# Performance work log

Measured on AMD Instinct MI355X. Metric: run time of the kernel, lower is better.

The kernel has to match this reference:

```python
import jax, jax.numpy as jnp
import numpy as np

BETA = 0.01  # soft-threshold level (init kwarg)
EPS = 1e-12


def vector_to_toeplitz(v):
    # v: [2N-1] complex generator; T[i, j] = v[N-1 + i - j], shape [N, N]
    n = (v.shape[0] + 1) // 2
    ii = jnp.arange(n)[:, None]
    jj = jnp.arange(n)[None, :]
    return v[(n - 1) + ii - jj]


def soft_thresh(z, beta):
    # complex soft-threshold (proximal op of beta*||.||_1):
    # z * max(|z| - beta, 0) / |z|
    mag = jnp.abs(z)
    scale = jnp.maximum(mag - beta, 0.0) / jnp.maximum(mag, EPS)
    return z * scale.astype(z.real.dtype)


def setup_inputs() -> dict:
    key = jax.random.key(0)
    ks = jax.random.split(key, 8)
    N, M, B = 1024, 256, 1024
    d = jnp.float32
    return {
        "v_re": jax.random.normal(ks[0], (2 * N - 1,), d),
        "v_im": jax.random.normal(ks[1], (2 * N - 1,), d),
        "W2_re": jax.random.normal(ks[2], (N, M), d) / np.sqrt(M),
        "W2_im": jax.random.normal(ks[3], (N, M), d) / np.sqrt(M),
        "x_re": jax.random.normal(ks[4], (N, B), d),
        "x_im": jax.random.normal(ks[5], (N, B), d),
        "y_re": jax.random.normal(ks[6], (M, B), d),
        "y_im": jax.random.normal(ks[7], (M, B), d),
    }


def reference(v_re, v_im, W2_re, W2_im, x_re, x_im, y_re, y_im):
    v = jax.lax.complex(v_re, v_im)      # [2N-1]
    W2 = jax.lax.complex(W2_re, W2_im)   # [N, M] (= A^H)
    x = jax.lax.complex(x_re, x_im)      # [N, B]
    y = jax.lax.complex(y_re, y_im)      # [M, B]
    W1 = vector_to_toeplitz(v)           # [N, N] Toeplitz
    # tpm(W1, x) + W2 @ y, then complex soft-threshold
    z = soft_thresh(W1 @ x + W2 @ y, BETA)  # [N, B]
    return z
```

## Files before the change

### kernel.cpp

```cpp
#include <hip/hip_runtime.h>
#include <hip/hip_fp16.h>
#include <cstdint>
#include <cstddef>


#define K_DIM 2560
#define BETA_F 0.01f
#define EPS_F  1e-12f

typedef __attribute__((ext_vector_type(8))) _Float16 half8;
typedef __attribute__((ext_vector_type(4))) _Float16 half4;
typedef __attribute__((ext_vector_type(4))) float   floatx4;

__device__ alignas(16) _Float16 g_Ap[1024 * K_DIM];
__device__ alignas(16) _Float16 g_Bt[2048 * K_DIM];
__device__ alignas(16) float    g_P0[1024 * 2048];
__device__ alignas(16) float    g_P1[1024 * 2048];

__global__ __launch_bounds__(256) void build_A(
    const float* __restrict__ v_re, const float* __restrict__ v_im,
    const float* __restrict__ W2_re, const float* __restrict__ W2_im)
{
    int t = blockIdx.x * 256 + threadIdx.x;
    int i  = t / 320;
    int c  = t - i * 320;
    int kp = c * 8;
    half8 h;
    if (kp < 1024) {
#pragma unroll
        for (int j = 0; j < 8; ++j) h[j] = (_Float16)v_re[1023 + i - kp - j];
    } else if (kp < 1280) {
        const float* s = W2_re + i * 256 + (kp - 1024);
#pragma unroll
        for (int j = 0; j < 8; ++j) h[j] = (_Float16)s[j];
    } else if (kp < 2304) {
        int k2 = kp - 1280;
#pragma unroll
        for (int j = 0; j < 8; ++j) h[j] = (_Float16)v_im[1023 + i - k2 - j];
    } else {
        const float* s = W2_im + i * 256 + (kp - 2304);
#pragma unroll
        for (int j = 0; j < 8; ++j) h[j] = (_Float16)s[j];
    }
    *reinterpret_cast<half8*>(g_Ap + (size_t)i * K_DIM + kp) = h;
}

__global__ __launch_bounds__(256) void build_Bt(
    const float* __restrict__ x_re, const float* __restrict__ x_im,
    const float* __restrict__ y_re, const float* __restrict__ y_im)
{
    __shared__ float lre[32][33];
    __shared__ float lim[32][33];
    int tid = threadIdx.x;
    int tx = tid & 31, ty = tid >> 5;
    int bx = blockIdx.x;
    const float* sre = (bx < 32) ? x_re : y_re;
    const float* sim = (bx < 32) ? x_im : y_im;
    int kb   = (bx < 32) ? bx : (bx - 32);
    int koff = (bx < 32) ? 0 : 1024;
    int k0 = kb * 32;
    int n0 = blockIdx.y * 32;
#pragma unroll
    for (int s = 0; s < 4; ++s) {
        int kk = ty + 8 * s;
        lre[kk][tx] = sre[(size_t)(k0 + kk) * 1024 + n0 + tx];
        lim[kk][tx] = sim[(size_t)(k0 + kk) * 1024 + n0 + tx];
    }
    __syncthreads();
    int lane_n = tid >> 3;
    int kq     = (tid & 7) * 4;
    half4 hre, him, hmim;
#pragma unroll
    for (int j = 0; j < 4; ++j) {
        float re = lre[kq + j][lane_n];
        float im = lim[kq + j][lane_n];
        hre[j]  = (_Float16)re;
        him[j]  = (_Float16)im;
        hmim[j] = (_Float16)(-im);
    }
    int n = n0 + lane_n;
    size_t kk2 = (size_t)koff + k0 + kq;
    _Float16* r0 = g_Bt + (size_t)(2 * n)     * K_DIM;
    _Float16* r1 = g_Bt + (size_t)(2 * n + 1) * K_DIM;
    *reinterpret_cast<half4*>(r0 + kk2)        = hre;
    *reinterpret_cast<half4*>(r0 + kk2 + 1280) = hmim;
    *reinterpret_cast<half4*>(r1 + kk2)        = him;
    *reinterpret_cast<half4*>(r1 + kk2 + 1280) = hre;
}

__global__ __launch_bounds__(256) void gemm_split(void)
{
    __shared__ __align__(16) _Float16 As[2 * 2 * 64 * 32];
    __shared__ __align__(16) _Float16 Bs[2 * 2 * 64 * 32];

    const int tid  = threadIdx.x;
    const int lane = tid & 63;
    const int w    = tid >> 6;
    const int wm   = w >> 1;
    const int wn   = w & 1;

    const int bid   = blockIdx.x;
    const int split = bid >> 9;
    const int sb    = bid & 511;
    const int xcd   = sb & 7;
    const int t     = sb >> 3;
    const int mi0 = ((xcd & 1) * 8 + (t & 7)) * 64;
    const int ni0 = ((xcd >> 1) * 8 + (t >> 3)) * 64;
    const int ks  = split * 1280;
    float* __restrict__ P = split ? g_P1 : g_P0;

    floatx4 acc[2][2];
#pragma unroll
    for (int a = 0; a < 2; ++a)
#pragma unroll
        for (int b = 0; b < 2; ++b) acc[a][b] = (floatx4)0.0f;

    const int rS = tid >> 2;
    const int jS = tid & 3;
    const int s0 = ((rS & 15) >> 1) & 3;
    char* asW = (char*)As + rS * 64 + ((jS ^ s0) * 16);
    char* bsW = (char*)Bs + rS * 64 + ((jS ^ s0) * 16);
    const _Float16* gA = g_Ap + (size_t)(mi0 + rS) * K_DIM + ks + jS * 8;
    const _Float16* gB = g_Bt + (size_t)(ni0 + rS) * K_DIM + ks + jS * 8;

    const int rowA = lane & 15;
    const int q    = lane >> 4;
    const int coff = (q ^ ((rowA >> 1) & 3)) * 16;

    {
        half8 pA0 = *reinterpret_cast<const half8*>(gA);
        half8 pA1 = *reinterpret_cast<const half8*>(gA + 32);
        half8 pB0 = *reinterpret_cast<const half8*>(gB);
        half8 pB1 = *reinterpret_cast<const half8*>(gB + 32);
        *reinterpret_cast<half8*>(asW)        = pA0;
        *reinterpret_cast<half8*>(asW + 4096) = pA1;
        *reinterpret_cast<half8*>(bsW)        = pB0;
        *reinterpret_cast<half8*>(bsW + 4096) = pB1;
    }
    __syncthreads();

    const int NIT = 1280 / 64;
    for (int kt = 0; kt < NIT; ++kt) {
        const int cur = kt & 1;
        half8 pA0, pA1, pB0, pB1;
        if (kt < NIT - 1) {
            const _Float16* ga = gA + (kt + 1) * 64;
            const _Float16* gb = gB + (kt + 1) * 64;
            pA0 = *reinterpret_cast<const half8*>(ga);
            pA1 = *reinterpret_cast<const half8*>(ga + 32);
            pB0 = *reinterpret_cast<const half8*>(gb);
            pB1 = *reinterpret_cast<const half8*>(gb + 32);
        }
        const char* Ab = (const char*)As + cur * 8192;
        const char* Bb = (const char*)Bs + cur * 8192;
        half8 af[2][2], bf[2][2];
#pragma unroll
        for (int mi = 0; mi < 2; ++mi) {
            int r = wm * 32 + mi * 16 + rowA;
            af[mi][0] = *reinterpret_cast<const half8*>(Ab + r * 64 + coff);
            af[mi][1] = *reinterpret_cast<const half8*>(Ab + 4096 + r * 64 + coff);
        }
#pragma unroll
        for (int ni = 0; ni < 2; ++ni) {
            int r = wn * 32 + ni * 16 + rowA;
            bf[ni][0] = *reinterpret_cast<const half8*>(Bb + r * 64 + coff);
            bf[ni][1] = *reinterpret_cast<const half8*>(Bb + 4096 + r * 64 + coff);
        }
#pragma unroll
        for (int mi = 0; mi < 2; ++mi)
#pragma unroll
            for (int ni = 0; ni < 2; ++ni) {
                acc[mi][ni] = __builtin_amdgcn_mfma_f32_16x16x32_f16(
                    af[mi][0], bf[ni][0], acc[mi][ni], 0, 0, 0);
                acc[mi][ni] = __builtin_amdgcn_mfma_f32_16x16x32_f16(
                    af[mi][1], bf[ni][1], acc[mi][ni], 0, 0, 0);
            }
        if (kt < NIT - 1) {
            char* aw = asW + (cur ^ 1) * 8192;
            char* bw = bsW + (cur ^ 1) * 8192;
            *reinterpret_cast<half8*>(aw)        = pA0;
            *reinterpret_cast<half8*>(aw + 4096) = pA1;
            *reinterpret_cast<half8*>(bw)        = pB0;
            *reinterpret_cast<half8*>(bw + 4096) = pB1;
        }
        __syncthreads();
    }

    const int colL  = lane & 15;
    const int rquad = (lane >> 4) * 4;
#pragma unroll
    for (int mi = 0; mi < 2; ++mi)
#pragma unroll
        for (int ni = 0; ni < 2; ++ni)
#pragma unroll
            for (int r = 0; r < 4; ++r) {
                int row = mi0 + wm * 32 + mi * 16 + rquad + r;
                int col = ni0 + wn * 32 + ni * 16 + colL;
                P[(size_t)row * 2048 + col] = acc[mi][ni][r];
            }
}

__global__ __launch_bounds__(256) void reduce_soft(float* __restrict__ out,
                                                   int out_n)
{
    int t = blockIdx.x * 256 + threadIdx.x;
    floatx4 v0 = reinterpret_cast<const floatx4*>(g_P0)[t];
    floatx4 v1 = reinterpret_cast<const floatx4*>(g_P1)[t];
    float re0 = v0[0] + v1[0], im0 = v0[1] + v1[1];
    float re1 = v0[2] + v1[2], im1 = v0[3] + v1[3];
    float m0 = sqrtf(re0 * re0 + im0 * im0);
    float m1 = sqrtf(re1 * re1 + im1 * im1);
    float s0 = fmaxf(m0 - BETA_F, 0.0f) / fmaxf(m0, EPS_F);
    float s1 = fmaxf(m1 - BETA_F, 0.0f) / fmaxf(m1, EPS_F);
    float2 r = make_float2(re0 * s0, re1 * s1);
    int idx = t * 2;
    if (idx + 1 < out_n)
        *reinterpret_cast<float2*>(out + idx) = r;
}

extern "C" void kernel_launch(void* const* d_in, const int* in_sizes, int n_in,
                              void* d_out, int out_size, void* d_ws, size_t ws_size,
                              hipStream_t stream) {
    (void)d_ws; (void)ws_size; (void)in_sizes; (void)n_in;
    const float* v_re  = (const float*)d_in[0];
    const float* v_im  = (const float*)d_in[1];
    const float* W2_re = (const float*)d_in[2];
    const float* W2_im = (const float*)d_in[3];
    const float* x_re  = (const float*)d_in[4];
    const float* x_im  = (const float*)d_in[5];
    const float* y_re  = (const float*)d_in[6];
    const float* y_im  = (const float*)d_in[7];
    float* out = (float*)d_out;

    build_A<<<1280, 256, 0, stream>>>(v_re, v_im, W2_re, W2_im);
    build_Bt<<<dim3(40, 32), 256, 0, stream>>>(x_re, x_im, y_re, y_im);
    gemm_split<<<1024, 256, 0, stream>>>();
    reduce_soft<<<2048, 256, 0, stream>>>(out, out_size);
}
```

Measured before the change: 116.9 us.

## Split GEMM K four ways, fuse build kernels, and add occupancy hint

Merges the two operand-building kernels into one launch, which removes one kernel boundary. The GEMM K dimension is split into four pieces instead of two, doubling the grid to 2048 blocks, and the block-to-tile mapping is reordered so that splits of the same tile land on the same XCD. A launch-bounds occupancy hint of 8 is also added. In exchange the partial-sum buffers double in size, so the reduce kernel must read four 8 MB arrays instead of two, which adds memory traffic.

```diff
diff --git a/kernel.cpp b/kernel.cpp
--- a/kernel.cpp
+++ b/kernel.cpp
@@ -14,52 +14,53 @@
 
 __device__ alignas(16) _Float16 g_Ap[1024 * K_DIM];
 __device__ alignas(16) _Float16 g_Bt[2048 * K_DIM];
-__device__ alignas(16) float    g_P0[1024 * 2048];
-__device__ alignas(16) float    g_P1[1024 * 2048];
-
-__global__ __launch_bounds__(256) void build_A(
+__device__ alignas(16) float    g_P[4][1024 * 2048];
+
+__global__ __launch_bounds__(256) void build_all(
     const float* __restrict__ v_re, const float* __restrict__ v_im,
-    const float* __restrict__ W2_re, const float* __restrict__ W2_im)
-{
-    int t = blockIdx.x * 256 + threadIdx.x;
-    int i  = t / 320;
-    int c  = t - i * 320;
-    int kp = c * 8;
-    half8 h;
-    if (kp < 1024) {
-#pragma unroll
-        for (int j = 0; j < 8; ++j) h[j] = (_Float16)v_re[1023 + i - kp - j];
-    } else if (kp < 1280) {
-        const float* s = W2_re + i * 256 + (kp - 1024);
-#pragma unroll
-        for (int j = 0; j < 8; ++j) h[j] = (_Float16)s[j];
-    } else if (kp < 2304) {
-        int k2 = kp - 1280;
-#pragma unroll
-        for (int j = 0; j < 8; ++j) h[j] = (_Float16)v_im[1023 + i - k2 - j];
-    } else {
-        const float* s = W2_im + i * 256 + (kp - 2304);
-#pragma unroll
-        for (int j = 0; j < 8; ++j) h[j] = (_Float16)s[j];
-    }
-    *reinterpret_cast<half8*>(g_Ap + (size_t)i * K_DIM + kp) = h;
-}
-
-__global__ __launch_bounds__(256) void build_Bt(
+    const float* __restrict__ W2_re, const float* __restrict__ W2_im,
     const float* __restrict__ x_re, const float* __restrict__ x_im,
     const float* __restrict__ y_re, const float* __restrict__ y_im)
 {
+    const int bx = blockIdx.x;
+    if (bx < 1280) {
+        int t = bx * 256 + threadIdx.x;
+        int i  = t / 320;
+        int c  = t - i * 320;
+        int kp = c * 8;
+        half8 h;
+        if (kp < 1024) {
+#pragma unroll
+            for (int j = 0; j < 8; ++j) h[j] = (_Float16)v_re[1023 + i - kp - j];
+        } else if (kp < 1280) {
+            const float* s = W2_re + i * 256 + (kp - 1024);
+#pragma unroll
+            for (int j = 0; j < 8; ++j) h[j] = (_Float16)s[j];
+        } else if (kp < 2304) {
+            int k2 = kp - 1280;
+#pragma unroll
+            for (int j = 0; j < 8; ++j) h[j] = (_Float16)v_im[1023 + i - k2 - j];
+        } else {
+            const float* s = W2_im + i * 256 + (kp - 2304);
+#pragma unroll
+            for (int j = 0; j < 8; ++j) h[j] = (_Float16)s[j];
+        }
+        *reinterpret_cast<half8*>(g_Ap + (size_t)i * K_DIM + kp) = h;
+        return;
+    }
     __shared__ float lre[32][33];
     __shared__ float lim[32][33];
+    int idx = bx - 1280;
+    int bk  = idx % 40;
+    int by  = idx / 40;
+    const float* sre = (bk < 32) ? x_re : y_re;
+    const float* sim = (bk < 32) ? x_im : y_im;
+    int kb   = (bk < 32) ? bk : (bk - 32);
+    int koff = (bk < 32) ? 0 : 1024;
+    int k0 = kb * 32;
+    int n0 = by * 32;
     int tid = threadIdx.x;
     int tx = tid & 31, ty = tid >> 5;
-    int bx = blockIdx.x;
-    const float* sre = (bx < 32) ? x_re : y_re;
-    const float* sim = (bx < 32) ? x_im : y_im;
-    int kb   = (bx < 32) ? bx : (bx - 32);
-    int koff = (bx < 32) ? 0 : 1024;
-    int k0 = kb * 32;
-    int n0 = blockIdx.y * 32;
 #pragma unroll
     for (int s = 0; s < 4; ++s) {
         int kk = ty + 8 * s;
@@ -88,7 +89,7 @@
     *reinterpret_cast<half4*>(r1 + kk2 + 1280) = hre;
 }
 
-__global__ __launch_bounds__(256) void gemm_split(void)
+__global__ __launch_bounds__(256, 8) void gemm_split(void)
 {
     __shared__ __align__(16) _Float16 As[2 * 2 * 64 * 32];
     __shared__ __align__(16) _Float16 Bs[2 * 2 * 64 * 32];
@@ -100,14 +101,14 @@
     const int wn   = w & 1;
 
     const int bid   = blockIdx.x;
-    const int split = bid >> 9;
-    const int sb    = bid & 511;
-    const int xcd   = sb & 7;
-    const int t     = sb >> 3;
-    const int mi0 = ((xcd & 1) * 8 + (t & 7)) * 64;
-    const int ni0 = ((xcd >> 1) * 8 + (t >> 3)) * 64;
-    const int ks  = split * 1280;
-    float* __restrict__ P = split ? g_P1 : g_P0;
+    const int xcd   = bid & 7;
+    const int t     = bid >> 3;
+    const int split = t & 3;
+    const int tile  = t >> 2;
+    const int mi0 = ((xcd & 1) * 8 + (tile & 7)) * 64;
+    const int ni0 = ((xcd >> 1) * 8 + (tile >> 3)) * 64;
+    const int ks  = split * 640;
+    float* __restrict__ P = g_P[split];
 
     floatx4 acc[2][2];
 #pragma unroll
@@ -139,7 +140,7 @@
     }
     __syncthreads();
 
-    const int NIT = 1280 / 64;
+    const int NIT = 640 / 64;
     for (int kt = 0; kt < NIT; ++kt) {
         const int cur = kt & 1;
         half8 pA0, pA1, pB0, pB1;
@@ -204,10 +205,14 @@
                                                    int out_n)
 {
     int t = blockIdx.x * 256 + threadIdx.x;
-    floatx4 v0 = reinterpret_cast<const floatx4*>(g_P0)[t];
-    floatx4 v1 = reinterpret_cast<const floatx4*>(g_P1)[t];
-    float re0 = v0[0] + v1[0], im0 = v0[1] + v1[1];
-    float re1 = v0[2] + v1[2], im1 = v0[3] + v1[3];
+    floatx4 v0 = reinterpret_cast<const floatx4*>(g_P[0])[t];
+    floatx4 v1 = reinterpret_cast<const floatx4*>(g_P[1])[t];
+    floatx4 v2 = reinterpret_cast<const floatx4*>(g_P[2])[t];
+    floatx4 v3 = reinterpret_cast<const floatx4*>(g_P[3])[t];
+    float re0 = (v0[0] + v1[0]) + (v2[0] + v3[0]);
+    float im0 = (v0[1] + v1[1]) + (v2[1] + v3[1]);
+    float re1 = (v0[2] + v1[2]) + (v2[2] + v3[2]);
+    float im1 = (v0[3] + v1[3]) + (v2[3] + v3[3]);
     float m0 = sqrtf(re0 * re0 + im0 * im0);
     float m1 = sqrtf(re1 * re1 + im1 * im1);
     float s0 = fmaxf(m0 - BETA_F, 0.0f) / fmaxf(m0, EPS_F);
@@ -232,8 +237,8 @@
     const float* y_im  = (const float*)d_in[7];
     float* out = (float*)d_out;
 
-    build_A<<<1280, 256, 0, stream>>>(v_re, v_im, W2_re, W2_im);
-    build_Bt<<<dim3(40, 32), 256, 0, stream>>>(x_re, x_im, y_re, y_im);
-    gemm_split<<<1024, 256, 0, stream>>>();
+    build_all<<<2560, 256, 0, stream>>>(v_re, v_im, W2_re, W2_im,
+                                        x_re, x_im, y_re, y_im);
+    gemm_split<<<2048, 256, 0, stream>>>();
     reduce_soft<<<2048, 256, 0, stream>>>(out, out_size);
 }
```

Measured after the change: 122.6 us. +4.9%, slower.
